# Kernel optimization log

Measured on AMD Instinct MI355X. Metric: run time of the kernel, lower is better.

Reference implementation:

```python
import jax, jax.numpy as jnp
import numpy as np

N_NODES = 10000
N_EDGES = 640000
IN_CH = 128
HID_CH = 128


def setup_inputs() -> dict:
    key = jax.random.key(0)
    ks = jax.random.split(key, 6)
    x = jax.random.normal(ks[0], (N_NODES, IN_CH), dtype=jnp.float32)
    edge_index = jax.random.randint(ks[1], (2, N_EDGES), 0, N_NODES, dtype=jnp.int32)
    # GCNConv weights (glorot-ish scale) and biases
    W1 = jax.random.normal(ks[2], (IN_CH, HID_CH), dtype=jnp.float32) / np.float32(np.sqrt(IN_CH))
    b1 = jnp.zeros((HID_CH,), jnp.float32)
    W2 = jax.random.normal(ks[3], (HID_CH, HID_CH), dtype=jnp.float32) / np.float32(np.sqrt(HID_CH))
    b2 = jnp.zeros((HID_CH,), jnp.float32)
    prelu_a = jnp.full((HID_CH,), 0.25, jnp.float32)  # nn.PReLU(hidden) init
    return {"x": x, "edge_index": edge_index, "W1": W1, "b1": b1,
            "W2": W2, "b2": b2, "prelu_a": prelu_a}


def _gcn_conv(x, W, b, src, dst, norm, n_nodes):
    # x: [N, Fin] -> transform, gather by src, scale by sym-norm, scatter-add to dst
    h = x @ W                                   # [N, Fout]
    msg = h[src] * norm[:, None]                # [E+N, Fout] gather (irregular)
    out = jax.ops.segment_sum(msg, dst, num_segments=n_nodes)
    return out + b


def reference(x, edge_index, W1, b1, W2, b2, prelu_a):
    n = x.shape[0]
    # PyG GCNConv default: add self-loops, symmetric D^{-1/2} A D^{-1/2} norm
    loops = jnp.arange(n, dtype=edge_index.dtype)
    src = jnp.concatenate([edge_index[0], loops])
    dst = jnp.concatenate([edge_index[1], loops])
    deg = jax.ops.segment_sum(jnp.ones_like(dst, dtype=jnp.float32), dst,
                              num_segments=n)
    dinv = jax.lax.rsqrt(jnp.maximum(deg, 1.0))  # deg >= 1 due to self-loops
    norm = dinv[src] * dinv[dst]                 # [E+N]

    h = _gcn_conv(x, W1, b1, src, dst, norm, n)
    h = jnp.where(h > 0, h, prelu_a * h)         # per-channel PReLU
    # Dropout(p=0.1) is identity in eval mode (correctness baseline)
    out = _gcn_conv(h, W2, b2, src, dst, norm, n)
    return out
```

## Files before the change

kernel.cpp:

```cpp
#include <hip/hip_runtime.h>

#define CH 128
#define HALF_CAP 96
#define ROW_ENT 192
#define CSTRIDE 32

typedef float    fvec4 __attribute__((ext_vector_type(4)));
typedef unsigned uvec4 __attribute__((ext_vector_type(4)));
typedef unsigned uvec2 __attribute__((ext_vector_type(2)));

__device__ __forceinline__ unsigned short f2bf(float f) {
    union { float f; unsigned int u; } v; v.f = f;
    unsigned int u = v.u;
    u += 0x7FFFu + ((u >> 16) & 1u);
    return (unsigned short)(u >> 16);
}
__device__ __forceinline__ float bflo(unsigned int p) {
    union { unsigned int u; float f; } v; v.u = p << 16; return v.f;
}
__device__ __forceinline__ float bfhi(unsigned int p) {
    union { unsigned int u; float f; } v; v.u = p & 0xFFFF0000u; return v.f;
}


__global__ void fill_slots_kernel(const int* __restrict__ src, const int* __restrict__ dst,
                                  int* __restrict__ cursor, unsigned short* __restrict__ slots,
                                  int E) {
    int e = blockIdx.x * blockDim.x + threadIdx.x;
    if (e < E) {
        int d = __builtin_nontemporal_load(dst + e);
        int s = __builtin_nontemporal_load(src + e);
        int p = e & 1;
        int r = atomicAdd(&cursor[((size_t)d * 2 + p) * CSTRIDE], 1);
        if (r < HALF_CAP)
            slots[(size_t)d * ROW_ENT + p * HALF_CAP + r] = (unsigned short)s;
    }
}

#define GTM 32
__global__ __launch_bounds__(256) void gemm_kernel(const float* __restrict__ A,
                                                   const float* __restrict__ W,
                                                   const int* __restrict__ deg,
                                                   float* __restrict__ C,
                                                   unsigned short* __restrict__ Cb,
                                                   int M) {
    __shared__ float Ws[128 * 128];
    int t = threadIdx.x;
    fvec4* Ws4 = (fvec4*)Ws;
    const fvec4* Wg = (const fvec4*)W;
#pragma unroll
    for (int i = 0; i < 16; ++i) Ws4[t + i * 256] = Wg[t + i * 256];
    __syncthreads();

    int rg = t >> 4, cg = t & 15;
    int row0 = blockIdx.x * GTM + rg * 2;
    const fvec4* Ar[2];
    bool val[2];
#pragma unroll
    for (int r = 0; r < 2; ++r) {
        int rr = row0 + r;
        val[r] = rr < M;
        Ar[r] = (const fvec4*)(A + (size_t)(val[r] ? rr : 0) * CH);
    }
    fvec4 acc[2][2];
#pragma unroll
    for (int r = 0; r < 2; ++r) {
        acc[r][0] = (fvec4){0.f, 0.f, 0.f, 0.f};
        acc[r][1] = (fvec4){0.f, 0.f, 0.f, 0.f};
    }
#pragma unroll 4
    for (int k4 = 0; k4 < 32; ++k4) {
        fvec4 a[2];
#pragma unroll
        for (int r = 0; r < 2; ++r) a[r] = Ar[r][k4];
#pragma unroll
        for (int j = 0; j < 4; ++j) {
            int k = k4 * 4 + j;
            fvec4 w0 = Ws4[k * 32 + cg];
            fvec4 w1 = Ws4[k * 32 + 16 + cg];
#pragma unroll
            for (int r = 0; r < 2; ++r) {
                float ar = a[r][j];
                acc[r][0] += ar * w0;
                acc[r][1] += ar * w1;
            }
        }
    }
#pragma unroll
    for (int r = 0; r < 2; ++r) {
        if (!val[r]) continue;
        int rr = row0 + r;
        int c0 = deg[(size_t)rr * 2 * CSTRIDE];
        int c1 = deg[((size_t)rr * 2 + 1) * CSTRIDE];
        float dn = rsqrtf((float)(c0 + c1 + 1));
        fvec4* C4 = (fvec4*)(C + (size_t)rr * CH);
        C4[cg] = acc[r][0];
        C4[16 + cg] = acc[r][1];
        fvec4 s0 = acc[r][0], s1 = acc[r][1];
        ushort4* B4 = (ushort4*)(Cb + (size_t)rr * CH);
        B4[cg]      = make_ushort4(f2bf(dn * s0.x), f2bf(dn * s0.y),
                                   f2bf(dn * s0.z), f2bf(dn * s0.w));
        B4[16 + cg] = make_ushort4(f2bf(dn * s1.x), f2bf(dn * s1.y),
                                   f2bf(dn * s1.z), f2bf(dn * s1.w));
    }
}

__global__ __launch_bounds__(256) void agg_kernel(const unsigned short* __restrict__ hb,
                                                  const float* __restrict__ hf,
                                                  const unsigned short* __restrict__ slots,
                                                  const int* __restrict__ deg,
                                                  const float* __restrict__ bias,
                                                  const float* __restrict__ prelu_a,
                                                  float* __restrict__ out,
                                                  int N, int apply_prelu) {
    int wave = threadIdx.x >> 6, lane = threadIdx.x & 63;
    int node = blockIdx.x * 4 + wave;
    if (node >= N) return;
    int half = lane >> 5;
    int sl = lane & 31;
    int dgh = deg[((size_t)node * 2 + half) * CSTRIDE];
    int dtot = dgh + __shfl_xor(dgh, 32);
    if (dgh > HALF_CAP) dgh = HALF_CAP;
    const unsigned short* sp = slots + (size_t)node * ROW_ENT + half * HALF_CAP;
    const unsigned short* hbl = hb + 4 * sl;
    float a0 = 0.f, a1 = 0.f, a2 = 0.f, a3 = 0.f;
    int k = 0;
    for (; k + 16 <= dgh; k += 16) {
        uvec4 qa = *(const uvec4*)(sp + k);
        uvec4 qb = *(const uvec4*)(sp + k + 8);
        unsigned q[8] = {qa.x, qa.y, qa.z, qa.w, qb.x, qb.y, qb.z, qb.w};
        uvec2 p[16];
#pragma unroll
        for (int j = 0; j < 8; ++j) {
            unsigned lo = q[j] & 0xFFFFu, hi = q[j] >> 16;
            p[2 * j]     = *(const uvec2*)(hbl + (size_t)lo * CH);
            p[2 * j + 1] = *(const uvec2*)(hbl + (size_t)hi * CH);
        }
#pragma unroll
        for (int j = 0; j < 16; ++j) {
            a0 += bflo(p[j].x); a1 += bfhi(p[j].x);
            a2 += bflo(p[j].y); a3 += bfhi(p[j].y);
        }
    }
    if (k < dgh) {
        uvec4 qa = *(const uvec4*)(sp + k);
        uvec4 qb = *(const uvec4*)(sp + k + 8);
        unsigned q[8] = {qa.x, qa.y, qa.z, qa.w, qb.x, qb.y, qb.z, qb.w};
#pragma unroll
        for (int j = 0; j < 8; ++j) {
            unsigned lo = q[j] & 0xFFFFu, hi = q[j] >> 16;
            lo = lo < (unsigned)N ? lo : 0u;
            hi = hi < (unsigned)N ? hi : 0u;
            uvec2 plo = *(const uvec2*)(hbl + (size_t)lo * CH);
            uvec2 phi = *(const uvec2*)(hbl + (size_t)hi * CH);
            if (k + 2 * j < dgh) {
                a0 += bflo(plo.x); a1 += bfhi(plo.x);
                a2 += bflo(plo.y); a3 += bfhi(plo.y);
            }
            if (k + 2 * j + 1 < dgh) {
                a0 += bflo(phi.x); a1 += bfhi(phi.x);
                a2 += bflo(phi.y); a3 += bfhi(phi.y);
            }
        }
    }
    a0 += __shfl_xor(a0, 32);
    a1 += __shfl_xor(a1, 32);
    a2 += __shfl_xor(a2, 32);
    a3 += __shfl_xor(a3, 32);
    if (half == 0) {
        float dn = rsqrtf((float)(dtot + 1));
        float d2 = dn * dn;
        fvec4 hv = ((const fvec4*)(hf + (size_t)node * CH))[sl];
        fvec4 bv = ((const fvec4*)bias)[sl];
        float r0 = dn * a0 + d2 * hv.x + bv.x;
        float r1 = dn * a1 + d2 * hv.y + bv.y;
        float r2 = dn * a2 + d2 * hv.z + bv.z;
        float r3 = dn * a3 + d2 * hv.w + bv.w;
        if (apply_prelu) {
            fvec4 av = ((const fvec4*)prelu_a)[sl];
            r0 = r0 > 0.f ? r0 : av.x * r0;
            r1 = r1 > 0.f ? r1 : av.y * r1;
            r2 = r2 > 0.f ? r2 : av.z * r2;
            r3 = r3 > 0.f ? r3 : av.w * r3;
        }
        fvec4 rv = {r0, r1, r2, r3};
        ((fvec4*)(out + (size_t)node * CH))[sl] = rv;
    }
}


extern "C" void kernel_launch(void* const* d_in, const int* in_sizes, int n_in,
                              void* d_out, int out_size, void* d_ws, size_t ws_size,
                              hipStream_t stream) {
    const float* x  = (const float*)d_in[0];
    const int*   ei = (const int*)d_in[1];
    const float* W1 = (const float*)d_in[2];
    const float* b1 = (const float*)d_in[3];
    const float* W2 = (const float*)d_in[4];
    const float* b2 = (const float*)d_in[5];
    const float* pa = (const float*)d_in[6];

    const int N = in_sizes[0] / CH;
    const int E = in_sizes[1] / 2;
    const int* src = ei;
    const int* dst = ei + E;

    char* w = (char*)d_ws;
    auto alloc = [&](size_t bytes) {
        void* p = (void*)w;
        w += (bytes + 255) & ~(size_t)255;
        return p;
    };
    int*            cursor = (int*)alloc((size_t)N * 2 * CSTRIDE * 4);
    unsigned short* slots  = (unsigned short*)alloc((size_t)N * ROW_ENT * 2);
    float*          bufA   = (float*)alloc((size_t)N * CH * 4);
    unsigned short* bufAb  = (unsigned short*)alloc((size_t)N * CH * 2);
    float*          bufB   = (float*)alloc((size_t)N * CH * 4);

    hipMemsetAsync(cursor, 0, (size_t)N * 2 * CSTRIDE * 4, stream);

    fill_slots_kernel<<<(E + 255) / 256, 256, 0, stream>>>(src, dst, cursor, slots, E);

    gemm_kernel<<<(N + GTM - 1) / GTM, 256, 0, stream>>>(x, W1, cursor, bufA, bufAb, N);
    agg_kernel<<<(N + 3) / 4, 256, 0, stream>>>(bufAb, bufA, slots, cursor, b1, pa, bufB, N, 1);
    gemm_kernel<<<(N + GTM - 1) / GTM, 256, 0, stream>>>(bufB, W2, cursor, bufA, bufAb, N);
    agg_kernel<<<(N + 3) / 4, 256, 0, stream>>>(bufAb, bufA, slots, cursor, b2, pa, (float*)d_out, N, 0);
}
```

Measured before the change: 169.9 us.

## Fuse GCN pipeline into one cooperative persistent kernel with grid syncs

Replaces the memset plus five separate launches with a single cooperative kernel of 512 blocks that uses grid-wide syncs between phases. The first GEMM runs on some blocks while the rest build the slot lists at the same time, and a separate scale phase converts to bf16 once the degrees are known. The goal is to remove launch gaps and overlap the atomic scatter with the first GEMM. The cost is several grid-wide barriers, persistent-loop scheduling of the aggregation, and a cooperative launch that must fit 512x512 threads with 64KB of shared memory each; it falls back to the old path if that launch fails.

```diff
diff --git a/kernel.cpp b/kernel.cpp
--- a/kernel.cpp
+++ b/kernel.cpp
@@ -1,11 +1,19 @@
 #include <hip/hip_runtime.h>
+#include <hip/hip_cooperative_groups.h>
+
+namespace cg = cooperative_groups;
 
 #define CH 128
 #define HALF_CAP 96
 #define ROW_ENT 192
 #define CSTRIDE 32
+#define NBLK 512
+#define NTHR 512
+#define SPLIT 160
+#define GTM 64
 
 typedef float    fvec4 __attribute__((ext_vector_type(4)));
+typedef float    fvec2 __attribute__((ext_vector_type(2)));
 typedef unsigned uvec4 __attribute__((ext_vector_type(4)));
 typedef unsigned uvec2 __attribute__((ext_vector_type(2)));
 
@@ -20,6 +28,211 @@
 }
 __device__ __forceinline__ float bfhi(unsigned int p) {
     union { unsigned int u; float f; } v; v.u = p & 0xFFFF0000u; return v.f;
+}
+
+
+__device__ __forceinline__ void gemm_phase(const float* __restrict__ A,
+                                           const float* __restrict__ W,
+                                           float* __restrict__ C,
+                                           unsigned short* __restrict__ Cb,
+                                           const int* __restrict__ cursor,
+                                           int premult, int M, int bid, int nB,
+                                           float* Ws) {
+    int ntiles = (M + GTM - 1) / GTM;
+    if (bid >= ntiles) return;
+    int t = threadIdx.x;
+    fvec4* Ws4 = (fvec4*)Ws;
+    const fvec4* Wg = (const fvec4*)W;
+#pragma unroll
+    for (int i = 0; i < 8; ++i) Ws4[t + i * NTHR] = Wg[t + i * NTHR];
+    __syncthreads();
+    int rg = t >> 4, cg = t & 15;
+    for (int tile = bid; tile < ntiles; tile += nB) {
+        int row0 = tile * GTM + rg * 2;
+        bool v0 = row0 < M, v1 = row0 + 1 < M;
+        const fvec4* Ar0 = (const fvec4*)(A + (size_t)(v0 ? row0 : 0) * CH);
+        const fvec4* Ar1 = (const fvec4*)(A + (size_t)(v1 ? row0 + 1 : 0) * CH);
+        fvec4 a00 = {0.f,0.f,0.f,0.f}, a01 = {0.f,0.f,0.f,0.f};
+        fvec4 a10 = {0.f,0.f,0.f,0.f}, a11 = {0.f,0.f,0.f,0.f};
+#pragma unroll 4
+        for (int k4 = 0; k4 < 32; ++k4) {
+            fvec4 a0 = Ar0[k4], a1 = Ar1[k4];
+#pragma unroll
+            for (int j = 0; j < 4; ++j) {
+                fvec4 w0 = Ws4[(k4 * 4 + j) * 32 + cg];
+                fvec4 w1 = Ws4[(k4 * 4 + j) * 32 + 16 + cg];
+                float e0 = a0[j], e1 = a1[j];
+                a00 += e0 * w0; a01 += e0 * w1;
+                a10 += e1 * w0; a11 += e1 * w1;
+            }
+        }
+#pragma unroll
+        for (int r = 0; r < 2; ++r) {
+            bool v = r ? v1 : v0;
+            if (!v) continue;
+            int rr = row0 + r;
+            fvec4 s0 = r ? a10 : a00, s1 = r ? a11 : a01;
+            fvec4* C4 = (fvec4*)(C + (size_t)rr * CH);
+            C4[cg] = s0;
+            C4[16 + cg] = s1;
+            if (premult) {
+                int c0 = cursor[(size_t)rr * 2 * CSTRIDE];
+                int c1 = cursor[((size_t)rr * 2 + 1) * CSTRIDE];
+                float dn = rsqrtf((float)(c0 + c1 + 1));
+                ushort4* B4 = (ushort4*)(Cb + (size_t)rr * CH);
+                B4[cg]      = make_ushort4(f2bf(dn * s0.x), f2bf(dn * s0.y),
+                                           f2bf(dn * s0.z), f2bf(dn * s0.w));
+                B4[16 + cg] = make_ushort4(f2bf(dn * s1.x), f2bf(dn * s1.y),
+                                           f2bf(dn * s1.z), f2bf(dn * s1.w));
+            }
+        }
+    }
+}
+
+__device__ __forceinline__ void scale_phase(const float* __restrict__ C,
+                                            const int* __restrict__ cursor,
+                                            unsigned short* __restrict__ Cb, int N) {
+    int wv = blockIdx.x * (NTHR / 64) + (threadIdx.x >> 6);
+    int lane = threadIdx.x & 63;
+    int nw = gridDim.x * (NTHR / 64);
+    for (int row = wv; row < N; row += nw) {
+        int c0 = cursor[(size_t)row * 2 * CSTRIDE];
+        int c1 = cursor[((size_t)row * 2 + 1) * CSTRIDE];
+        float dn = rsqrtf((float)(c0 + c1 + 1));
+        fvec2 v = ((const fvec2*)(C + (size_t)row * CH))[lane];
+        unsigned pk = ((unsigned)f2bf(dn * v.y) << 16) | (unsigned)f2bf(dn * v.x);
+        ((unsigned*)(Cb + (size_t)row * CH))[lane] = pk;
+    }
+}
+
+__device__ void agg_phase(const unsigned short* __restrict__ hb,
+                          const float* __restrict__ hf,
+                          const unsigned short* __restrict__ slots,
+                          const int* __restrict__ cursor,
+                          const float* __restrict__ bias,
+                          const float* __restrict__ prelu_a,
+                          float* __restrict__ outp,
+                          int N, int apply_prelu) {
+    int wave = threadIdx.x >> 6, lane = threadIdx.x & 63;
+    int half = lane >> 5, sl = lane & 31;
+    int gw = blockIdx.x * (NTHR / 64) + wave;
+    int nw = gridDim.x * (NTHR / 64);
+    const unsigned short* hbl = hb + 4 * sl;
+    fvec4 bv = ((const fvec4*)bias)[sl];
+    fvec4 av = ((const fvec4*)prelu_a)[sl];
+    for (int node = gw; node < N; node += nw) {
+        int dgh = cursor[((size_t)node * 2 + half) * CSTRIDE];
+        int dtot = dgh + __shfl_xor(dgh, 32);
+        if (dgh > HALF_CAP) dgh = HALF_CAP;
+        const unsigned short* sp = slots + (size_t)node * ROW_ENT + half * HALF_CAP;
+        float a0 = 0.f, a1 = 0.f, a2 = 0.f, a3 = 0.f;
+        int k = 0;
+        for (; k + 16 <= dgh; k += 16) {
+            uvec4 qa = *(const uvec4*)(sp + k);
+            uvec4 qb = *(const uvec4*)(sp + k + 8);
+            unsigned q[8] = {qa.x, qa.y, qa.z, qa.w, qb.x, qb.y, qb.z, qb.w};
+            uvec2 p[16];
+#pragma unroll
+            for (int j = 0; j < 8; ++j) {
+                unsigned lo = q[j] & 0xFFFFu, hi = q[j] >> 16;
+                p[2 * j]     = *(const uvec2*)(hbl + (size_t)lo * CH);
+                p[2 * j + 1] = *(const uvec2*)(hbl + (size_t)hi * CH);
+            }
+#pragma unroll
+            for (int j = 0; j < 16; ++j) {
+                a0 += bflo(p[j].x); a1 += bfhi(p[j].x);
+                a2 += bflo(p[j].y); a3 += bfhi(p[j].y);
+            }
+        }
+        if (k < dgh) {
+            uvec4 qa = *(const uvec4*)(sp + k);
+            uvec4 qb = *(const uvec4*)(sp + k + 8);
+            unsigned q[8] = {qa.x, qa.y, qa.z, qa.w, qb.x, qb.y, qb.z, qb.w};
+#pragma unroll
+            for (int j = 0; j < 8; ++j) {
+                unsigned lo = q[j] & 0xFFFFu, hi = q[j] >> 16;
+                lo = lo < (unsigned)N ? lo : 0u;
+                hi = hi < (unsigned)N ? hi : 0u;
+                uvec2 plo = *(const uvec2*)(hbl + (size_t)lo * CH);
+                uvec2 phi = *(const uvec2*)(hbl + (size_t)hi * CH);
+                if (k + 2 * j < dgh) {
+                    a0 += bflo(plo.x); a1 += bfhi(plo.x);
+                    a2 += bflo(plo.y); a3 += bfhi(plo.y);
+                }
+                if (k + 2 * j + 1 < dgh) {
+                    a0 += bflo(phi.x); a1 += bfhi(phi.x);
+                    a2 += bflo(phi.y); a3 += bfhi(phi.y);
+                }
+            }
+        }
+        a0 += __shfl_xor(a0, 32);
+        a1 += __shfl_xor(a1, 32);
+        a2 += __shfl_xor(a2, 32);
+        a3 += __shfl_xor(a3, 32);
+        if (half == 0) {
+            float dn = rsqrtf((float)(dtot + 1));
+            float d2 = dn * dn;
+            fvec4 hv = ((const fvec4*)(hf + (size_t)node * CH))[sl];
+            float r0 = dn * a0 + d2 * hv.x + bv.x;
+            float r1 = dn * a1 + d2 * hv.y + bv.y;
+            float r2 = dn * a2 + d2 * hv.z + bv.z;
+            float r3 = dn * a3 + d2 * hv.w + bv.w;
+            if (apply_prelu) {
+                r0 = r0 > 0.f ? r0 : av.x * r0;
+                r1 = r1 > 0.f ? r1 : av.y * r1;
+                r2 = r2 > 0.f ? r2 : av.z * r2;
+                r3 = r3 > 0.f ? r3 : av.w * r3;
+            }
+            fvec4 rv = {r0, r1, r2, r3};
+            ((fvec4*)(outp + (size_t)node * CH))[sl] = rv;
+        }
+    }
+}
+
+
+__global__ __launch_bounds__(NTHR, 4) void fused_kernel(
+    const float* __restrict__ x, const int* __restrict__ src, const int* __restrict__ dst,
+    const float* __restrict__ W1, const float* __restrict__ b1,
+    const float* __restrict__ W2, const float* __restrict__ b2,
+    const float* __restrict__ pa,
+    int* __restrict__ cursor, unsigned short* __restrict__ slots,
+    float* __restrict__ bufA, unsigned short* __restrict__ bufAb,
+    float* __restrict__ bufB, float* __restrict__ outp,
+    int N, int E) {
+    __shared__ float Ws[128 * 128];
+    cg::grid_group grid = cg::this_grid();
+    int bid = blockIdx.x, t = threadIdx.x;
+
+    int total = N * 2 * CSTRIDE;
+    for (int i = bid * NTHR + t; i < total; i += gridDim.x * NTHR) cursor[i] = 0;
+    grid.sync();
+
+    if (bid < SPLIT) {
+        gemm_phase(x, W1, bufA, nullptr, cursor, 0, N, bid, SPLIT, Ws);
+    } else {
+        int ft = (bid - SPLIT) * NTHR + t;
+        int fstride = (gridDim.x - SPLIT) * NTHR;
+        for (int e = ft; e < E; e += fstride) {
+            int d = __builtin_nontemporal_load(dst + e);
+            int s = __builtin_nontemporal_load(src + e);
+            int p = e & 1;
+            int r = atomicAdd(&cursor[((size_t)d * 2 + p) * CSTRIDE], 1);
+            if (r < HALF_CAP)
+                slots[(size_t)d * ROW_ENT + p * HALF_CAP + r] = (unsigned short)s;
+        }
+    }
+    grid.sync();
+
+    scale_phase(bufA, cursor, bufAb, N);
+    grid.sync();
+
+    agg_phase(bufAb, bufA, slots, cursor, b1, pa, bufB, N, 1);
+    grid.sync();
+
+    gemm_phase(bufB, W2, bufA, bufAb, cursor, 1, N, bid, gridDim.x, Ws);
+    grid.sync();
+
+    agg_phase(bufAb, bufA, slots, cursor, b2, pa, outp, N, 0);
 }
 
 
@@ -37,7 +250,6 @@
     }
 }
 
-#define GTM 32
 __global__ __launch_bounds__(256) void gemm_kernel(const float* __restrict__ A,
                                                    const float* __restrict__ W,
                                                    const int* __restrict__ deg,
@@ -51,52 +263,37 @@
 #pragma unroll
     for (int i = 0; i < 16; ++i) Ws4[t + i * 256] = Wg[t + i * 256];
     __syncthreads();
-
     int rg = t >> 4, cg = t & 15;
-    int row0 = blockIdx.x * GTM + rg * 2;
-    const fvec4* Ar[2];
-    bool val[2];
-#pragma unroll
-    for (int r = 0; r < 2; ++r) {
-        int rr = row0 + r;
-        val[r] = rr < M;
-        Ar[r] = (const fvec4*)(A + (size_t)(val[r] ? rr : 0) * CH);
-    }
-    fvec4 acc[2][2];
-#pragma unroll
-    for (int r = 0; r < 2; ++r) {
-        acc[r][0] = (fvec4){0.f, 0.f, 0.f, 0.f};
-        acc[r][1] = (fvec4){0.f, 0.f, 0.f, 0.f};
-    }
+    int row0 = blockIdx.x * 32 + rg * 2;
+    bool v0 = row0 < M, v1 = row0 + 1 < M;
+    const fvec4* Ar0 = (const fvec4*)(A + (size_t)(v0 ? row0 : 0) * CH);
+    const fvec4* Ar1 = (const fvec4*)(A + (size_t)(v1 ? row0 + 1 : 0) * CH);
+    fvec4 a00 = {0.f,0.f,0.f,0.f}, a01 = {0.f,0.f,0.f,0.f};
+    fvec4 a10 = {0.f,0.f,0.f,0.f}, a11 = {0.f,0.f,0.f,0.f};
 #pragma unroll 4
     for (int k4 = 0; k4 < 32; ++k4) {
-        fvec4 a[2];
-#pragma unroll
-        for (int r = 0; r < 2; ++r) a[r] = Ar[r][k4];
+        fvec4 a0 = Ar0[k4], a1 = Ar1[k4];
 #pragma unroll
         for (int j = 0; j < 4; ++j) {
-            int k = k4 * 4 + j;
-            fvec4 w0 = Ws4[k * 32 + cg];
-            fvec4 w1 = Ws4[k * 32 + 16 + cg];
-#pragma unroll
-            for (int r = 0; r < 2; ++r) {
-                float ar = a[r][j];
-                acc[r][0] += ar * w0;
-                acc[r][1] += ar * w1;
-            }
+            fvec4 w0 = Ws4[(k4 * 4 + j) * 32 + cg];
+            fvec4 w1 = Ws4[(k4 * 4 + j) * 32 + 16 + cg];
+            float e0 = a0[j], e1 = a1[j];
+            a00 += e0 * w0; a01 += e0 * w1;
+            a10 += e1 * w0; a11 += e1 * w1;
         }
     }
 #pragma unroll
     for (int r = 0; r < 2; ++r) {
-        if (!val[r]) continue;
+        bool v = r ? v1 : v0;
+        if (!v) continue;
         int rr = row0 + r;
+        fvec4 s0 = r ? a10 : a00, s1 = r ? a11 : a01;
         int c0 = deg[(size_t)rr * 2 * CSTRIDE];
         int c1 = deg[((size_t)rr * 2 + 1) * CSTRIDE];
         float dn = rsqrtf((float)(c0 + c1 + 1));
         fvec4* C4 = (fvec4*)(C + (size_t)rr * CH);
-        C4[cg] = acc[r][0];
-        C4[16 + cg] = acc[r][1];
-        fvec4 s0 = acc[r][0], s1 = acc[r][1];
+        C4[cg] = s0;
+        C4[16 + cg] = s1;
         ushort4* B4 = (ushort4*)(Cb + (size_t)rr * CH);
         B4[cg]      = make_ushort4(f2bf(dn * s0.x), f2bf(dn * s0.y),
                                    f2bf(dn * s0.z), f2bf(dn * s0.w));
@@ -108,17 +305,16 @@
 __global__ __launch_bounds__(256) void agg_kernel(const unsigned short* __restrict__ hb,
                                                   const float* __restrict__ hf,
                                                   const unsigned short* __restrict__ slots,
-                                                  const int* __restrict__ deg,
+                                                  const int* __restrict__ cursor,
                                                   const float* __restrict__ bias,
                                                   const float* __restrict__ prelu_a,
-                                                  float* __restrict__ out,
+                                                  float* __restrict__ outp,
                                                   int N, int apply_prelu) {
     int wave = threadIdx.x >> 6, lane = threadIdx.x & 63;
     int node = blockIdx.x * 4 + wave;
     if (node >= N) return;
-    int half = lane >> 5;
-    int sl = lane & 31;
-    int dgh = deg[((size_t)node * 2 + half) * CSTRIDE];
+    int half = lane >> 5, sl = lane & 31;
+    int dgh = cursor[((size_t)node * 2 + half) * CSTRIDE];
     int dtot = dgh + __shfl_xor(dgh, 32);
     if (dgh > HALF_CAP) dgh = HALF_CAP;
     const unsigned short* sp = slots + (size_t)node * ROW_ENT + half * HALF_CAP;
@@ -184,7 +380,7 @@
             r3 = r3 > 0.f ? r3 : av.w * r3;
         }
         fvec4 rv = {r0, r1, r2, r3};
-        ((fvec4*)(out + (size_t)node * CH))[sl] = rv;
+        ((fvec4*)(outp + (size_t)node * CH))[sl] = rv;
     }
 }
 
@@ -200,8 +396,8 @@
     const float* b2 = (const float*)d_in[5];
     const float* pa = (const float*)d_in[6];
 
-    const int N = in_sizes[0] / CH;
-    const int E = in_sizes[1] / 2;
+    int N = in_sizes[0] / CH;
+    int E = in_sizes[1] / 2;
     const int* src = ei;
     const int* dst = ei + E;
 
@@ -216,13 +412,19 @@
     float*          bufA   = (float*)alloc((size_t)N * CH * 4);
     unsigned short* bufAb  = (unsigned short*)alloc((size_t)N * CH * 2);
     float*          bufB   = (float*)alloc((size_t)N * CH * 4);
-
-    hipMemsetAsync(cursor, 0, (size_t)N * 2 * CSTRIDE * 4, stream);
-
-    fill_slots_kernel<<<(E + 255) / 256, 256, 0, stream>>>(src, dst, cursor, slots, E);
-
-    gemm_kernel<<<(N + GTM - 1) / GTM, 256, 0, stream>>>(x, W1, cursor, bufA, bufAb, N);
-    agg_kernel<<<(N + 3) / 4, 256, 0, stream>>>(bufAb, bufA, slots, cursor, b1, pa, bufB, N, 1);
-    gemm_kernel<<<(N + GTM - 1) / GTM, 256, 0, stream>>>(bufB, W2, cursor, bufA, bufAb, N);
-    agg_kernel<<<(N + 3) / 4, 256, 0, stream>>>(bufAb, bufA, slots, cursor, b2, pa, (float*)d_out, N, 0);
-}
+    float*          outp   = (float*)d_out;
+
+    void* args[] = {&x, &src, &dst, &W1, &b1, &W2, &b2, &pa,
+                    &cursor, &slots, &bufA, &bufAb, &bufB, &outp, &N, &E};
+    hipError_t rc = hipLaunchCooperativeKernel((const void*)fused_kernel,
+                                               dim3(NBLK), dim3(NTHR), args, 0, stream);
+    if (rc != hipSuccess) {
+        (void)hipGetLastError();
+        hipMemsetAsync(cursor, 0, (size_t)N * 2 * CSTRIDE * 4, stream);
+        fill_slots_kernel<<<(E + 255) / 256, 256, 0, stream>>>(src, dst, cursor, slots, E);
+        gemm_kernel<<<(N + 31) / 32, 256, 0, stream>>>(x, W1, cursor, bufA, bufAb, N);
+        agg_kernel<<<(N + 3) / 4, 256, 0, stream>>>(bufAb, bufA, slots, cursor, b1, pa, bufB, N, 1);
+        gemm_kernel<<<(N + 31) / 32, 256, 0, stream>>>(bufB, W2, cursor, bufA, bufAb, N);
+        agg_kernel<<<(N + 3) / 4, 256, 0, stream>>>(bufAb, bufA, slots, cursor, b2, pa, outp, N, 0);
+    }
+}
```

Result: slower. 460.0 us (+170.7%).
